# Kernel optimization log

Measured on AMD Instinct MI355X. Metric: run time of the kernel, lower is better.

The kernel has to match this reference:

```python
import jax, jax.numpy as jnp
import numpy as np

H = 16           # num_heads
D = 1024         # hidden_size
HD = D // H      # head_dim = 64
LN_EPS = 1e-5


def setup_inputs() -> dict:
    key = jax.random.key(0)
    ks = jax.random.split(key, 11)
    s = 1.0 / np.sqrt(D)
    x = jax.random.normal(ks[0], (2, 2048, D), dtype=jnp.float32)
    Wq = jax.random.uniform(ks[1], (D, D), jnp.float32, -s, s)
    bq = jax.random.uniform(ks[2], (D,), jnp.float32, -s, s)
    Wk = jax.random.uniform(ks[3], (D, D), jnp.float32, -s, s)
    bk = jax.random.uniform(ks[4], (D,), jnp.float32, -s, s)
    Wv = jax.random.uniform(ks[5], (D, D), jnp.float32, -s, s)
    bv = jax.random.uniform(ks[6], (D,), jnp.float32, -s, s)
    Wo = jax.random.uniform(ks[7], (D, D), jnp.float32, -s, s)
    bo = jax.random.uniform(ks[8], (D,), jnp.float32, -s, s)
    gamma = jnp.ones((D,), jnp.float32)
    beta = jnp.zeros((D,), jnp.float32)
    return {"x": x, "Wq": Wq, "bq": bq, "Wk": Wk, "bk": bk,
            "Wv": Wv, "bv": bv, "Wo": Wo, "bo": bo,
            "gamma": gamma, "beta": beta}


def reference(x, Wq, bq, Wk, bk, Wv, bv, Wo, bo, gamma, beta):
    B, S, _ = x.shape
    # projections -> [B, H, S, HD]
    def split_heads(t):
        return t.reshape(B, S, H, HD).transpose(0, 2, 1, 3)
    Q = split_heads(x @ Wq + bq)
    K = split_heads(x @ Wk + bk)
    V = split_heads(x @ Wv + bv)
    # scores [B, H, S, S], softmax over keys (dropout = identity in eval)
    scores = jnp.einsum('bhqd,bhkd->bhqk', Q, K) / np.sqrt(HD).astype(np.float32)
    attn = jax.nn.softmax(scores, axis=-1)
    ctx = jnp.einsum('bhqk,bhkd->bhqd', attn, V)          # [B, H, S, HD]
    ctx = ctx.transpose(0, 2, 1, 3).reshape(B, S, H * HD)  # [B, S, D]
    out = ctx @ Wo + bo
    # residual + LayerNorm
    y = out + x
    mu = jnp.mean(y, axis=-1, keepdims=True)
    var = jnp.mean(jnp.square(y - mu), axis=-1, keepdims=True)
    return (y - mu) * jax.lax.rsqrt(var + LN_EPS) * gamma + beta
```

## Files before the change

### kernel.cpp

```cpp
#include <hip/hip_runtime.h>
#include <cstdint>
#include <cstddef>


typedef short  b16x8  __attribute__((ext_vector_type(8)));
typedef float  f32x4  __attribute__((ext_vector_type(4)));
typedef float  f32x16 __attribute__((ext_vector_type(16)));

#define AS1 __attribute__((address_space(1)))
#define AS3 __attribute__((address_space(3)))

__device__ __forceinline__ unsigned short f2bf(float f) {
    unsigned int u = __builtin_bit_cast(unsigned int, f);
    u += 0x7FFFu + ((u >> 16) & 1u);
    return (unsigned short)(u >> 16);
}

__device__ __forceinline__ unsigned int cvt_pk_bf16(float lo, float hi) {
    unsigned int r;
    asm("v_cvt_pk_bf16_f32 %0, %1, %2" : "=v"(r) : "v"(lo), "v"(hi));
    return r;
}

__device__ __forceinline__ float exp2_fast(float x) {
    float r;
    asm("v_exp_f32 %0, %1" : "=v"(r) : "v"(x));
    return r;
}

__device__ __forceinline__ void permswap(unsigned &a, unsigned &b) {
    asm volatile("v_permlane32_swap_b32 %0, %1" : "+v"(a), "+v"(b));
}

__global__ __launch_bounds__(256) void k_cvt_x(const float* __restrict__ x,
                                               unsigned short* __restrict__ xb) {
    int i = blockIdx.x * 256 + threadIdx.x;
    float4 v = ((const float4*)x)[i];
    ushort4 o;
    o.x = f2bf(v.x); o.y = f2bf(v.y); o.z = f2bf(v.z); o.w = f2bf(v.w);
    ((ushort4*)xb)[i] = o;
}

__global__ __launch_bounds__(1024) void k_cvt_w(
    const float* __restrict__ W0, const float* __restrict__ W1,
    const float* __restrict__ W2, const float* __restrict__ W3,
    unsigned short* __restrict__ T0, unsigned short* __restrict__ T1,
    unsigned short* __restrict__ T2, unsigned short* __restrict__ T3) {
    const float* W = blockIdx.z == 0 ? W0 : blockIdx.z == 1 ? W1 : blockIdx.z == 2 ? W2 : W3;
    unsigned short* T = blockIdx.z == 0 ? T0 : blockIdx.z == 1 ? T1 : blockIdx.z == 2 ? T2 : T3;
    __shared__ float tile[32][33];
    int k0 = blockIdx.x * 32, n0 = blockIdx.y * 32;
    int tx = threadIdx.x, ty = threadIdx.y;
    tile[ty][tx] = W[(size_t)(k0 + ty) * 1024 + n0 + tx];
    __syncthreads();
    T[(size_t)(n0 + ty) * 1024 + k0 + tx] = f2bf(tile[tx][ty]);
}

__global__ __launch_bounds__(512) void k_gemm_qkv(
    const unsigned short* __restrict__ A, const unsigned short* __restrict__ Bt,
    const float* __restrict__ bq, const float* __restrict__ bk, const float* __restrict__ bv,
    unsigned short* __restrict__ Qb, unsigned short* __restrict__ Kt,
    unsigned short* __restrict__ Vt) {
    __shared__ unsigned short As[2][256 * 32];
    __shared__ unsigned short Bs[2][96 * 32];
    const int tid = threadIdx.x, lane = tid & 63, wid = tid >> 6;
    const int m0 = blockIdx.y * 256, n0 = blockIdx.x * 96;
    const int wr = wid >> 1, wc = wid & 1;
    f32x4 acc[4][3] = {};

    const int srow = tid >> 2, scol = (tid & 3) * 8;
    const unsigned short* Ag  = A  + (size_t)(m0 + srow) * 1024 + scol;
    const unsigned short* Ag2 = A  + (size_t)(m0 + 128 + srow) * 1024 + scol;
    const unsigned short* Bg  = Bt + (size_t)(n0 + srow) * 1024 + scol;

#define GSTAGE(kt, buf) do {                                                              \
        __builtin_amdgcn_global_load_lds((const AS1 void*)(Ag  + (kt) * 32),              \
                                         (AS3 void*)((char*)As[buf] + tid * 16),        16, 0, 0); \
        __builtin_amdgcn_global_load_lds((const AS1 void*)(Ag2 + (kt) * 32),              \
                                         (AS3 void*)((char*)As[buf] + 8192 + tid * 16), 16, 0, 0); \
        if (tid < 384)                                                                    \
            __builtin_amdgcn_global_load_lds((const AS1 void*)(Bg + (kt) * 32),           \
                                             (AS3 void*)((char*)Bs[buf] + tid * 16),    16, 0, 0); \
    } while (0)

    GSTAGE(0, 0);
    __syncthreads();

    const int g = lane >> 4, r = lane & 15;
    for (int kt = 0; kt < 32; ++kt) {
        const int cur = kt & 1;
        if (kt < 31) GSTAGE(kt + 1, cur ^ 1);
        b16x8 af[4], bfr[3];
#pragma unroll
        for (int mi = 0; mi < 4; ++mi)
            af[mi] = __builtin_bit_cast(b16x8, *(const uint4*)(As[cur] + (wr * 64 + mi * 16 + r) * 32 + g * 8));
#pragma unroll
        for (int ni = 0; ni < 3; ++ni)
            bfr[ni] = __builtin_bit_cast(b16x8, *(const uint4*)(Bs[cur] + (wc * 48 + ni * 16 + r) * 32 + g * 8));
#pragma unroll
        for (int mi = 0; mi < 4; ++mi)
#pragma unroll
            for (int ni = 0; ni < 3; ++ni)
                acc[mi][ni] = __builtin_amdgcn_mfma_f32_16x16x32_bf16(af[mi], bfr[ni], acc[mi][ni], 0, 0, 0);
        __syncthreads();
    }
#undef GSTAGE

    for (int ni = 0; ni < 3; ++ni) {
        int col = n0 + wc * 48 + ni * 16 + r;
        int which = col >> 10, c = col & 1023;
        const float* bp = which == 0 ? bq : which == 1 ? bk : bv;
        float bvv = bp[c];
        int h = c >> 6, hd = c & 63;
        for (int mi = 0; mi < 4; ++mi)
            for (int j = 0; j < 4; ++j) {
                int row = m0 + wr * 64 + mi * 16 + g * 4 + j;
                float v = acc[mi][ni][j] + bvv;
                int b = row >> 11, s = row & 2047;
                size_t bh = (size_t)(b * 16 + h);
                if (which == 0) {
                    Qb[(bh * 2048 + s) * 64 + hd] = f2bf(v * 0.180336881f);
                } else if (which == 1) {
                    int tt = s >> 6, kr = s & 63;
                    Kt[(bh * 32 + tt) * 4096 + ((kr * 64 + hd) ^ ((kr & 7) << 3))] = f2bf(v);
                } else {
                    int tt = s >> 6, cc = s & 63;
                    Vt[(bh * 32 + tt) * 4096 + ((hd * 64 + cc) ^ ((hd & 7) << 3))] = f2bf(v);
                }
            }
    }
}

__global__ __launch_bounds__(512) void k_gemm_proj(
    const unsigned short* __restrict__ A, const unsigned short* __restrict__ Bt,
    const float* __restrict__ bias, float* __restrict__ out) {
    __shared__ unsigned short As[2][128 * 32];
    __shared__ unsigned short Bs[2][64 * 32];
    const int tid = threadIdx.x, lane = tid & 63, wid = tid >> 6;
    const int m0 = blockIdx.y * 128, n0 = blockIdx.x * 64;
    const int wr = wid >> 1, wc = wid & 1;
    f32x4 acc[2][2] = {};

    const int srow = tid >> 2, scol = (tid & 3) * 8;
    const unsigned short* Ag = A  + (size_t)(m0 + srow) * 1024 + scol;
    const unsigned short* Bg = Bt + (size_t)(n0 + srow) * 1024 + scol;

#define PSTAGE(kt, buf) do {                                                              \
        __builtin_amdgcn_global_load_lds((const AS1 void*)(Ag + (kt) * 32),               \
                                         (AS3 void*)((char*)As[buf] + tid * 16), 16, 0, 0); \
        if (tid < 256)                                                                    \
            __builtin_amdgcn_global_load_lds((const AS1 void*)(Bg + (kt) * 32),           \
                                             (AS3 void*)((char*)Bs[buf] + tid * 16), 16, 0, 0); \
    } while (0)

    PSTAGE(0, 0);
    __syncthreads();

    const int g = lane >> 4, r = lane & 15;
    for (int kt = 0; kt < 32; ++kt) {
        const int cur = kt & 1;
        if (kt < 31) PSTAGE(kt + 1, cur ^ 1);
        b16x8 af[2], bfr[2];
#pragma unroll
        for (int mi = 0; mi < 2; ++mi)
            af[mi] = __builtin_bit_cast(b16x8, *(const uint4*)(As[cur] + (wr * 32 + mi * 16 + r) * 32 + g * 8));
#pragma unroll
        for (int ni = 0; ni < 2; ++ni)
            bfr[ni] = __builtin_bit_cast(b16x8, *(const uint4*)(Bs[cur] + (wc * 32 + ni * 16 + r) * 32 + g * 8));
#pragma unroll
        for (int mi = 0; mi < 2; ++mi)
#pragma unroll
            for (int ni = 0; ni < 2; ++ni)
                acc[mi][ni] = __builtin_amdgcn_mfma_f32_16x16x32_bf16(af[mi], bfr[ni], acc[mi][ni], 0, 0, 0);
        __syncthreads();
    }
#undef PSTAGE

    for (int mi = 0; mi < 2; ++mi)
        for (int ni = 0; ni < 2; ++ni) {
            int col = n0 + wc * 32 + ni * 16 + r;
            float bv = bias[col];
            for (int j = 0; j < 4; ++j) {
                int row = m0 + wr * 32 + mi * 16 + g * 4 + j;
                out[(size_t)row * 1024 + col] = acc[mi][ni][j] + bv;
            }
        }
}

#define TSWZ(row, byteoff) ((((row) * 128) + (byteoff)) ^ (((row) & 7) << 4))

__global__ __launch_bounds__(512, 4) void k_attn(const unsigned short* __restrict__ Qb,
                                                 const unsigned short* __restrict__ Kt,
                                                 const unsigned short* __restrict__ Vt,
                                                 unsigned short* __restrict__ ctx) {
    __shared__ unsigned short Ks[2][2][4096];
    __shared__ unsigned short Vs[2][2][4096];
    __shared__ float lsh[4][64];
    const int tid = threadIdx.x, lane = tid & 63, w = tid >> 6;
    const int q32 = lane & 31, hi = lane >> 5;
    const int wq = w & 3, grp = w >> 2;
    const int lt = wq * 64 + lane;

    int bid = blockIdx.x;
    int xcd = bid & 7, idx = bid >> 3;
    int bh = xcd * 4 + (idx & 3);
    int q0 = (idx >> 2) * 128;
    const int b = bh >> 4, h = bh & 15;

    const unsigned short* qrow = Qb + ((size_t)bh * 2048 + q0 + wq * 32 + q32) * 64 + hi * 8;
    b16x8 qf[4];
#pragma unroll
    for (int ds = 0; ds < 4; ++ds)
        qf[ds] = __builtin_bit_cast(b16x8, *(const uint4*)(qrow + ds * 16));

    const unsigned short* Kg = Kt + (size_t)bh * 32 * 4096;
    const unsigned short* Vg = Vt + (size_t)bh * 32 * 4096;
    const int ktbase = grp * 16;

#define STAGE(i, buf) do {                                                                \
        const unsigned short* _ks = Kg + (size_t)(ktbase + (i)) * 4096 + lt * 8;          \
        const unsigned short* _vs = Vg + (size_t)(ktbase + (i)) * 4096 + lt * 8;          \
        __builtin_amdgcn_global_load_lds((const AS1 void*)_ks,          (AS3 void*)((char*)Ks[grp][buf] + lt * 16),        16, 0, 0); \
        __builtin_amdgcn_global_load_lds((const AS1 void*)(_ks + 2048), (AS3 void*)((char*)Ks[grp][buf] + 4096 + lt * 16), 16, 0, 0); \
        __builtin_amdgcn_global_load_lds((const AS1 void*)_vs,          (AS3 void*)((char*)Vs[grp][buf] + lt * 16),        16, 0, 0); \
        __builtin_amdgcn_global_load_lds((const AS1 void*)(_vs + 2048), (AS3 void*)((char*)Vs[grp][buf] + 4096 + lt * 16), 16, 0, 0); \
    } while (0)

    float lpart = 0.f;
    f32x16 oacc[2] = {};

    STAGE(0, 0);
    __syncthreads();

    for (int i = 0; i < 16; ++i) {
        const int cur = i & 1;
        if (i < 15) STAGE(i + 1, cur ^ 1);

        f32x16 sacc[2] = {};
#pragma unroll
        for (int ds = 0; ds < 4; ++ds) {
            b16x8 kf0 = __builtin_bit_cast(b16x8, *(const uint4*)((char*)Ks[grp][cur] + TSWZ(q32,      ds * 32 + hi * 16)));
            b16x8 kf1 = __builtin_bit_cast(b16x8, *(const uint4*)((char*)Ks[grp][cur] + TSWZ(32 + q32, ds * 32 + hi * 16)));
            sacc[0] = __builtin_amdgcn_mfma_f32_32x32x16_bf16(kf0, qf[ds], sacc[0], 0, 0, 0);
            sacc[1] = __builtin_amdgcn_mfma_f32_32x32x16_bf16(kf1, qf[ds], sacc[1], 0, 0, 0);
        }

        float pb[2][16];
#pragma unroll
        for (int kb = 0; kb < 2; ++kb)
#pragma unroll
            for (int reg = 0; reg < 16; ++reg)
                pb[kb][reg] = exp2_fast(sacc[kb][reg]);
        {
            float t0 = (pb[0][0]  + pb[0][1])  + (pb[0][2]  + pb[0][3]);
            float t1 = (pb[0][4]  + pb[0][5])  + (pb[0][6]  + pb[0][7]);
            float t2 = (pb[0][8]  + pb[0][9])  + (pb[0][10] + pb[0][11]);
            float t3 = (pb[0][12] + pb[0][13]) + (pb[0][14] + pb[0][15]);
            float t4 = (pb[1][0]  + pb[1][1])  + (pb[1][2]  + pb[1][3]);
            float t5 = (pb[1][4]  + pb[1][5])  + (pb[1][6]  + pb[1][7]);
            float t6 = (pb[1][8]  + pb[1][9])  + (pb[1][10] + pb[1][11]);
            float t7 = (pb[1][12] + pb[1][13]) + (pb[1][14] + pb[1][15]);
            lpart += ((t0 + t1) + (t2 + t3)) + ((t4 + t5) + (t6 + t7));
        }
        unsigned wv[2][4][2];
#pragma unroll
        for (int kb = 0; kb < 2; ++kb)
#pragma unroll
            for (int rg = 0; rg < 4; ++rg) {
                wv[kb][rg][0] = cvt_pk_bf16(pb[kb][rg * 4 + 0], pb[kb][rg * 4 + 1]);
                wv[kb][rg][1] = cvt_pk_bf16(pb[kb][rg * 4 + 2], pb[kb][rg * 4 + 3]);
            }
        b16x8 pa[4];
#pragma unroll
        for (int ks = 0; ks < 4; ++ks) {
            int kb = ks >> 1, rg0 = (ks & 1) * 2;
            unsigned u0 = wv[kb][rg0][0], u2 = wv[kb][rg0 + 1][0];
            permswap(u0, u2);
            unsigned u1 = wv[kb][rg0][1], u3 = wv[kb][rg0 + 1][1];
            permswap(u1, u3);
            uint4 uu; uu.x = u0; uu.y = u1; uu.z = u2; uu.w = u3;
            pa[ks] = __builtin_bit_cast(b16x8, uu);
        }
#pragma unroll
        for (int ks = 0; ks < 4; ++ks) {
            b16x8 vf0 = __builtin_bit_cast(b16x8, *(const uint4*)((char*)Vs[grp][cur] + TSWZ(q32,      ks * 32 + hi * 16)));
            b16x8 vf1 = __builtin_bit_cast(b16x8, *(const uint4*)((char*)Vs[grp][cur] + TSWZ(32 + q32, ks * 32 + hi * 16)));
            oacc[0] = __builtin_amdgcn_mfma_f32_32x32x16_bf16(pa[ks], vf0, oacc[0], 0, 0, 0);
            oacc[1] = __builtin_amdgcn_mfma_f32_32x32x16_bf16(pa[ks], vf1, oacc[1], 0, 0, 0);
        }
        __syncthreads();
    }

    {
        unsigned a = __builtin_bit_cast(unsigned, lpart), bb = a;
        permswap(a, bb);
        lpart = __builtin_bit_cast(float, a) + __builtin_bit_cast(float, bb);
    }

    float* s0 = (float*)Ks[1];
    float* s1 = (float*)Vs[1];
    if (grp == 1) {
        int base = (wq * 64 + lane) * 16;
#pragma unroll
        for (int reg = 0; reg < 16; ++reg) {
            s0[base + reg] = oacc[0][reg];
            s1[base + reg] = oacc[1][reg];
        }
        lsh[wq][lane] = lpart;
    }
    __syncthreads();
    if (grp == 0) {
        float l = lpart + lsh[wq][lane];
        float inv = 1.f / l;
        int base = (wq * 64 + lane) * 16;
#pragma unroll
        for (int reg = 0; reg < 16; ++reg) {
            int qr = (reg & 3) + 8 * (reg >> 2) + 4 * hi;
            float iv = __shfl(inv, qr, 64);
            float o0 = (oacc[0][reg] + s0[base + reg]) * iv;
            float o1 = (oacc[1][reg] + s1[base + reg]) * iv;
            unsigned short* dst = ctx + ((size_t)(b * 2048 + q0 + wq * 32 + qr)) * 1024 + h * 64 + q32;
            dst[0]  = f2bf(o0);
            dst[32] = f2bf(o1);
        }
    }
#undef STAGE
}

__global__ __launch_bounds__(256) void k_ln(const float* __restrict__ proj,
                                            const float* __restrict__ x,
                                            const float* __restrict__ gamma,
                                            const float* __restrict__ beta,
                                            float* __restrict__ out) {
    int t = threadIdx.x, lane = t & 63, w = t >> 6;
    int row = blockIdx.x * 4 + w;
    const float4* pr = (const float4*)(proj + (size_t)row * 1024);
    const float4* xr = (const float4*)(x    + (size_t)row * 1024);
    float4 y[4];
    float s = 0.f, ss = 0.f;
#pragma unroll
    for (int i = 0; i < 4; ++i) {
        float4 a = pr[lane + i * 64], bx = xr[lane + i * 64];
        float4 yy;
        yy.x = a.x + bx.x; yy.y = a.y + bx.y; yy.z = a.z + bx.z; yy.w = a.w + bx.w;
        y[i] = yy;
        s  += yy.x + yy.y + yy.z + yy.w;
        ss += yy.x * yy.x + yy.y * yy.y + yy.z * yy.z + yy.w * yy.w;
    }
#pragma unroll
    for (int o = 32; o > 0; o >>= 1) {
        s  += __shfl_xor(s,  o, 64);
        ss += __shfl_xor(ss, o, 64);
    }
    float mu  = s * (1.f / 1024.f);
    float var = ss * (1.f / 1024.f) - mu * mu;
    float inv = rsqrtf(var + 1e-5f);
    float4* outr = (float4*)(out + (size_t)row * 1024);
    const float4* gr = (const float4*)gamma;
    const float4* br = (const float4*)beta;
#pragma unroll
    for (int i = 0; i < 4; ++i) {
        float4 g4 = gr[lane + i * 64], b4 = br[lane + i * 64];
        float4 o4;
        o4.x = (y[i].x - mu) * inv * g4.x + b4.x;
        o4.y = (y[i].y - mu) * inv * g4.y + b4.y;
        o4.z = (y[i].z - mu) * inv * g4.z + b4.z;
        o4.w = (y[i].w - mu) * inv * g4.w + b4.w;
        outr[lane + i * 64] = o4;
    }
}

extern "C" void kernel_launch(void* const* d_in, const int* in_sizes, int n_in,
                              void* d_out, int out_size, void* d_ws, size_t ws_size,
                              hipStream_t stream) {
    const float* x  = (const float*)d_in[0];
    const float* Wq = (const float*)d_in[1];
    const float* bq = (const float*)d_in[2];
    const float* Wk = (const float*)d_in[3];
    const float* bk = (const float*)d_in[4];
    const float* Wv = (const float*)d_in[5];
    const float* bv = (const float*)d_in[6];
    const float* Wo = (const float*)d_in[7];
    const float* bo = (const float*)d_in[8];
    const float* gamma = (const float*)d_in[9];
    const float* beta  = (const float*)d_in[10];

    char* ws = (char*)d_ws;
    const size_t MB = 1u << 20;
    unsigned short* xbf   = (unsigned short*)(ws);
    unsigned short* Wqkvt = (unsigned short*)(ws + 8 * MB);
    unsigned short* Wot   = (unsigned short*)(ws + 14 * MB);
    unsigned short* Qb    = (unsigned short*)(ws + 16 * MB);
    unsigned short* Kt    = (unsigned short*)(ws + 24 * MB);
    unsigned short* Vt    = (unsigned short*)(ws + 32 * MB);
    float* proj = (float*)(ws + 16 * MB);
    unsigned short* ctx = xbf;

    k_cvt_x<<<4096, 256, 0, stream>>>(x, xbf);
    k_cvt_w<<<dim3(32, 32, 4), dim3(32, 32), 0, stream>>>(
        Wq, Wk, Wv, Wo, Wqkvt, Wqkvt + 1024 * 1024, Wqkvt + 2 * 1024 * 1024, Wot);
    k_gemm_qkv<<<dim3(32, 16), 512, 0, stream>>>(xbf, Wqkvt, bq, bk, bv, Qb, Kt, Vt);
    k_attn<<<512, 512, 0, stream>>>(Qb, Kt, Vt, ctx);
    k_gemm_proj<<<dim3(16, 32), 512, 0, stream>>>(ctx, Wot, bo, proj);
    k_ln<<<1024, 256, 0, stream>>>(proj, x, gamma, beta, (float*)d_out);
}
```

Baseline: 131.6 us.

## Pre-tile and swizzle QKV GEMM operands; use 128x128 tiles with triple-buffered loads

The x and Wqkv conversion kernels now write bf16 data in 128x64 tiles with an XOR swizzle. This lets the QKV GEMM fetch each k-tile as one contiguous block straight into LDS, with reads free of bank conflicts. The GEMM moves from 256x96 tiles with k=32 to 128x128 tiles with k=64. It uses three LDS buffers with prefetch distance two and explicit vmcnt waits, which reduces barriers and hides load latency. In exchange it uses more LDS per block, which may lower occupancy, and runs a different grid of 768 blocks.

```diff
diff --git a/kernel.cpp b/kernel.cpp
--- a/kernel.cpp
+++ b/kernel.cpp
@@ -35,10 +35,16 @@
 __global__ __launch_bounds__(256) void k_cvt_x(const float* __restrict__ x,
                                                unsigned short* __restrict__ xb) {
     int i = blockIdx.x * 256 + threadIdx.x;
-    float4 v = ((const float4*)x)[i];
-    ushort4 o;
-    o.x = f2bf(v.x); o.y = f2bf(v.y); o.z = f2bf(v.z); o.w = f2bf(v.w);
-    ((ushort4*)xb)[i] = o;
+    size_t base = (size_t)i * 8;
+    float4 v0 = *(const float4*)(x + base);
+    float4 v1 = *(const float4*)(x + base + 4);
+    int row = (int)(base >> 10), col = (int)(base & 1023);
+    int rt = row >> 7, rr = row & 127, kt = col >> 6, cc = col & 63;
+    int e = (rr * 64 + cc) ^ ((rr & 7) << 3);
+    unsigned short o[8];
+    o[0] = f2bf(v0.x); o[1] = f2bf(v0.y); o[2] = f2bf(v0.z); o[3] = f2bf(v0.w);
+    o[4] = f2bf(v1.x); o[5] = f2bf(v1.y); o[6] = f2bf(v1.z); o[7] = f2bf(v1.w);
+    *(uint4*)(xb + (size_t)(rt * 16 + kt) * 8192 + e) = *(uint4*)o;
 }
 
 __global__ __launch_bounds__(1024) void k_cvt_w(
@@ -53,7 +59,15 @@
     int tx = threadIdx.x, ty = threadIdx.y;
     tile[ty][tx] = W[(size_t)(k0 + ty) * 1024 + n0 + tx];
     __syncthreads();
-    T[(size_t)(n0 + ty) * 1024 + k0 + tx] = f2bf(tile[tx][ty]);
+    int n = n0 + ty, k = k0 + tx;
+    unsigned short v = f2bf(tile[tx][ty]);
+    if (blockIdx.z == 3) {
+        T[(size_t)n * 1024 + k] = v;
+    } else {
+        int r = n & 127, c = k & 63;
+        int e = (r * 64 + c) ^ ((r & 7) << 3);
+        T[(size_t)((n >> 7) * 16 + (k >> 6)) * 8192 + e] = v;
+    }
 }
 
 __global__ __launch_bounds__(512) void k_gemm_qkv(
@@ -61,53 +75,69 @@
     const float* __restrict__ bq, const float* __restrict__ bk, const float* __restrict__ bv,
     unsigned short* __restrict__ Qb, unsigned short* __restrict__ Kt,
     unsigned short* __restrict__ Vt) {
-    __shared__ unsigned short As[2][256 * 32];
-    __shared__ unsigned short Bs[2][96 * 32];
+    __shared__ unsigned short As[3][8192];
+    __shared__ unsigned short Bs[3][8192];
     const int tid = threadIdx.x, lane = tid & 63, wid = tid >> 6;
-    const int m0 = blockIdx.y * 256, n0 = blockIdx.x * 96;
-    const int wr = wid >> 1, wc = wid & 1;
-    f32x4 acc[4][3] = {};
-
-    const int srow = tid >> 2, scol = (tid & 3) * 8;
-    const unsigned short* Ag  = A  + (size_t)(m0 + srow) * 1024 + scol;
-    const unsigned short* Ag2 = A  + (size_t)(m0 + 128 + srow) * 1024 + scol;
-    const unsigned short* Bg  = Bt + (size_t)(n0 + srow) * 1024 + scol;
+    const int m0 = blockIdx.y * 128, n0 = blockIdx.x * 128;
+    const int wr = wid >> 2, wc = wid & 3;
+    const int g = lane >> 4, r = lane & 15;
+    f32x4 acc[4][2] = {};
+
+    const unsigned short* Abase = A  + (size_t)blockIdx.y * 16 * 8192;
+    const unsigned short* Bbase = Bt + (size_t)blockIdx.x * 16 * 8192;
 
 #define GSTAGE(kt, buf) do {                                                              \
-        __builtin_amdgcn_global_load_lds((const AS1 void*)(Ag  + (kt) * 32),              \
-                                         (AS3 void*)((char*)As[buf] + tid * 16),        16, 0, 0); \
-        __builtin_amdgcn_global_load_lds((const AS1 void*)(Ag2 + (kt) * 32),              \
-                                         (AS3 void*)((char*)As[buf] + 8192 + tid * 16), 16, 0, 0); \
-        if (tid < 384)                                                                    \
-            __builtin_amdgcn_global_load_lds((const AS1 void*)(Bg + (kt) * 32),           \
-                                             (AS3 void*)((char*)Bs[buf] + tid * 16),    16, 0, 0); \
+        const unsigned short* _a = Abase + (size_t)(kt) * 8192 + tid * 8;                 \
+        const unsigned short* _b = Bbase + (size_t)(kt) * 8192 + tid * 8;                 \
+        __builtin_amdgcn_global_load_lds((const AS1 void*)(_a),        (AS3 void*)((char*)As[buf] + tid * 16),        16, 0, 0); \
+        __builtin_amdgcn_global_load_lds((const AS1 void*)(_a + 4096), (AS3 void*)((char*)As[buf] + 8192 + tid * 16), 16, 0, 0); \
+        __builtin_amdgcn_global_load_lds((const AS1 void*)(_b),        (AS3 void*)((char*)Bs[buf] + tid * 16),        16, 0, 0); \
+        __builtin_amdgcn_global_load_lds((const AS1 void*)(_b + 4096), (AS3 void*)((char*)Bs[buf] + 8192 + tid * 16), 16, 0, 0); \
     } while (0)
 
     GSTAGE(0, 0);
-    __syncthreads();
-
-    const int g = lane >> 4, r = lane & 15;
-    for (int kt = 0; kt < 32; ++kt) {
-        const int cur = kt & 1;
-        if (kt < 31) GSTAGE(kt + 1, cur ^ 1);
-        b16x8 af[4], bfr[3];
-#pragma unroll
-        for (int mi = 0; mi < 4; ++mi)
-            af[mi] = __builtin_bit_cast(b16x8, *(const uint4*)(As[cur] + (wr * 64 + mi * 16 + r) * 32 + g * 8));
-#pragma unroll
-        for (int ni = 0; ni < 3; ++ni)
-            bfr[ni] = __builtin_bit_cast(b16x8, *(const uint4*)(Bs[cur] + (wc * 48 + ni * 16 + r) * 32 + g * 8));
-#pragma unroll
-        for (int mi = 0; mi < 4; ++mi)
-#pragma unroll
-            for (int ni = 0; ni < 3; ++ni)
-                acc[mi][ni] = __builtin_amdgcn_mfma_f32_16x16x32_bf16(af[mi], bfr[ni], acc[mi][ni], 0, 0, 0);
-        __syncthreads();
+    GSTAGE(1, 1);
+    asm volatile("s_waitcnt vmcnt(4)" ::: "memory");
+    __builtin_amdgcn_s_barrier();
+    __builtin_amdgcn_sched_barrier(0);
+
+    for (int kt = 0; kt < 16; ++kt) {
+        const unsigned short* Ac = As[kt % 3];
+        const unsigned short* Bc = Bs[kt % 3];
+        if (kt < 14) GSTAGE(kt + 2, (kt + 2) % 3);
+#pragma unroll
+        for (int kk = 0; kk < 2; ++kk) {
+            b16x8 af[4], bfr[2];
+#pragma unroll
+            for (int mi = 0; mi < 4; ++mi) {
+                int row = wr * 64 + mi * 16 + r;
+                int e = (row * 64 + kk * 32 + g * 8) ^ ((row & 7) << 3);
+                af[mi] = __builtin_bit_cast(b16x8, *(const uint4*)(Ac + e));
+            }
+#pragma unroll
+            for (int ni = 0; ni < 2; ++ni) {
+                int row = wc * 32 + ni * 16 + r;
+                int e = (row * 64 + kk * 32 + g * 8) ^ ((row & 7) << 3);
+                bfr[ni] = __builtin_bit_cast(b16x8, *(const uint4*)(Bc + e));
+            }
+#pragma unroll
+            for (int mi = 0; mi < 4; ++mi)
+#pragma unroll
+                for (int ni = 0; ni < 2; ++ni)
+                    acc[mi][ni] = __builtin_amdgcn_mfma_f32_16x16x32_bf16(af[mi], bfr[ni], acc[mi][ni], 0, 0, 0);
+        }
+        asm volatile("s_waitcnt lgkmcnt(0)" ::: "memory");
+        if (kt < 15) {
+            if (kt < 14) asm volatile("s_waitcnt vmcnt(4)" ::: "memory");
+            else         asm volatile("s_waitcnt vmcnt(0)" ::: "memory");
+            __builtin_amdgcn_s_barrier();
+            __builtin_amdgcn_sched_barrier(0);
+        }
     }
 #undef GSTAGE
 
-    for (int ni = 0; ni < 3; ++ni) {
-        int col = n0 + wc * 48 + ni * 16 + r;
+    for (int ni = 0; ni < 2; ++ni) {
+        int col = n0 + wc * 32 + ni * 16 + r;
         int which = col >> 10, c = col & 1023;
         const float* bp = which == 0 ? bq : which == 1 ? bk : bv;
         float bvv = bp[c];
@@ -396,10 +426,10 @@
     float* proj = (float*)(ws + 16 * MB);
     unsigned short* ctx = xbf;
 
-    k_cvt_x<<<4096, 256, 0, stream>>>(x, xbf);
+    k_cvt_x<<<2048, 256, 0, stream>>>(x, xbf);
     k_cvt_w<<<dim3(32, 32, 4), dim3(32, 32), 0, stream>>>(
         Wq, Wk, Wv, Wo, Wqkvt, Wqkvt + 1024 * 1024, Wqkvt + 2 * 1024 * 1024, Wot);
-    k_gemm_qkv<<<dim3(32, 16), 512, 0, stream>>>(xbf, Wqkvt, bq, bk, bv, Qb, Kt, Vt);
+    k_gemm_qkv<<<dim3(24, 32), 512, 0, stream>>>(xbf, Wqkvt, bq, bk, bv, Qb, Kt, Vt);
     k_attn<<<512, 512, 0, stream>>>(Qb, Kt, Vt, ctx);
     k_gemm_proj<<<dim3(16, 32), 512, 0, stream>>>(ctx, Wot, bo, proj);
     k_ln<<<1024, 256, 0, stream>>>(proj, x, gamma, beta, (float*)d_out);
```

After: 128.8 us. 1.02x faster.
